# Performance work log

Hardware: AMD Instinct MI355X
Metric: run time of the kernel (lower is better)

Reference implementation:

```python
import jax, jax.numpy as jnp
import numpy as np

NUM_HEADS = 4
NUM_LEVELS = 4
NUM_POINTS = 8
EMBED = 256
HEAD_DIM = EMBED // NUM_HEADS
SHAPES = np.array([[92, 160], [46, 80], [23, 40], [12, 20]], dtype=np.int64)  # (h, w) per level
NUM_VALUE = int((SHAPES[:, 0] * SHAPES[:, 1]).sum())  # 19560
DEPTH = 64
NQ = 20000
BS = 1
NZ = 4  # num_Z_anchors; NUM_POINTS % NZ == 0


def _depth_bias():
    # replicates init_smpl_off_weights for sampling_offsets_depth.bias
    th = np.arange(NUM_HEADS) * (2.0 * np.pi / NUM_HEADS)
    g = ((np.cos(th) + np.sin(th)) / 2.0)[:, None, None] * np.ones((NUM_HEADS, NUM_LEVELS, NUM_POINTS))
    g = g * (np.arange(NUM_POINTS) + 1)[None, None, :]
    return jnp.asarray(g.reshape(-1), dtype=jnp.float32)


def setup_inputs() -> dict:
    key = jax.random.key(0)
    ks = jax.random.split(key, 8)
    f = jnp.float32
    s = 0.02
    query = jax.random.normal(ks[0], (BS, NQ, EMBED), f)
    value = jax.random.normal(ks[1], (BS, NUM_VALUE, EMBED), f)
    value_dpt_dist = jax.nn.softmax(jax.random.normal(ks[2], (BS, NUM_VALUE, DEPTH), f), axis=-1)
    reference_points = jax.random.uniform(ks[3], (BS, NQ, NZ, 3), f)
    spatial_shapes = jnp.asarray(SHAPES)
    level_start_index = jnp.asarray(np.concatenate([[0], np.cumsum(SHAPES[:, 0] * SHAPES[:, 1])[:-1]]))
    Wv = jax.random.normal(ks[4], (EMBED, EMBED), f) * s
    bv = jnp.zeros((EMBED,), f)
    Wo = jax.random.normal(ks[5], (EMBED, NUM_HEADS * NUM_LEVELS * NUM_POINTS * 2), f) * s
    bo = jax.random.normal(ks[6], (NUM_HEADS * NUM_LEVELS * NUM_POINTS * 2,), f) * 0.5
    Wod = jnp.zeros((EMBED, NUM_HEADS * NUM_LEVELS * NUM_POINTS), f)  # constant_init 0.0
    bod = _depth_bias()
    Wa = jax.random.normal(ks[7], (EMBED, NUM_HEADS * NUM_LEVELS * NUM_POINTS), f) * s
    ba = jnp.zeros((NUM_HEADS * NUM_LEVELS * NUM_POINTS,), f)
    return dict(query=query, value=value, value_dpt_dist=value_dpt_dist,
                reference_points=reference_points, spatial_shapes=spatial_shapes,
                level_start_index=level_start_index, Wv=Wv, bv=bv, Wo=Wo, bo=bo,
                Wod=Wod, bod=bod, Wa=Wa, ba=ba)


def _forward(query, value, value_dpt_dist, reference_points, spatial_shapes,
             level_start_index, Wv, bv, Wo, bo, Wod, bod, Wa, ba):
    bs, nq, _ = query.shape
    H, L, P = NUM_HEADS, NUM_LEVELS, NUM_POINTS
    dh = HEAD_DIM
    D = value_dpt_dist.shape[-1]
    dt = query.dtype
    shapes = np.asarray(spatial_shapes)  # static level shapes

    v = (value @ Wv + bv).reshape(bs, -1, H, dh)  # value_proj
    off_uv = (query @ Wo + bo).reshape(bs, nq, H, L, P, 2)
    off_d = (query @ Wod + bod).reshape(bs, nq, H, L, P, 1)
    off = jnp.concatenate([off_uv, off_d], axis=-1)  # (bs,nq,H,L,P,3)
    attn = jax.nn.softmax((query @ Wa + ba).reshape(bs, nq, H, L * P), axis=-1)
    attn = attn.reshape(bs, nq, H, L, P)

    # offset_normalizer = (w, h, D) per level
    norm = jnp.asarray(np.stack([shapes[:, 1], shapes[:, 0], np.full(L, D)], -1), dtype=dt)
    off = off / norm[None, None, None, :, None, :]
    Z = reference_points.shape[2]
    off = off.reshape(bs, nq, H, L, P // Z, Z, 3)
    loc = (reference_points[:, :, None, None, None, :, :] + off).reshape(bs, nq, H, L, P, 3)

    starts = np.concatenate([[0], np.cumsum(shapes[:, 0] * shapes[:, 1])]).astype(int)
    gather_bh = jax.vmap(jax.vmap(lambda a, i: a[i]))   # over (bs, heads)
    gather_b = jax.vmap(lambda a, i: a[i])              # over bs

    out = jnp.zeros((bs, nq, H, dh), dt)
    for l in range(L):
        Hl, Wl = int(shapes[l, 0]), int(shapes[l, 1])
        v_l = v[:, starts[l]:starts[l + 1]].transpose(0, 2, 1, 3)          # (bs,H,HW,dh)
        d_l = value_dpt_dist[:, starts[l]:starts[l + 1]].reshape(bs, Hl * Wl * D)
        ll = loc[:, :, :, l]                                               # (bs,nq,H,P,3)
        # grid_sample (align_corners=False) pixel coordinates
        x = ll[..., 0] * Wl - 0.5
        y = ll[..., 1] * Hl - 0.5
        z = ll[..., 2] * D - 0.5
        x0f, y0f, z0f = jnp.floor(x), jnp.floor(y), jnp.floor(z)
        fx, fy, fz = x - x0f, y - y0f, z - z0f
        x0 = x0f.astype(jnp.int32); y0 = y0f.astype(jnp.int32); z0 = z0f.astype(jnp.int32)
        z0c = jnp.clip(z0, 0, D - 1)
        z1c = jnp.clip(z0 + 1, 0, D - 1)
        wz0 = (1.0 - fz) * ((z0 >= 0) & (z0 <= D - 1)).astype(dt)
        wz1 = fz * ((z0 + 1 >= 0) & (z0 + 1 <= D - 1)).astype(dt)

        acc = jnp.zeros((bs, nq, H, P, dh), dt)
        for xi, wx in ((x0, 1.0 - fx), (x0 + 1, fx)):
            for yi, wy in ((y0, 1.0 - fy), (y0 + 1, fy)):
                valid = ((xi >= 0) & (xi < Wl) & (yi >= 0) & (yi < Hl)).astype(dt)
                w_uv = wx * wy * valid                                     # (bs,nq,H,P)
                idx = jnp.clip(yi, 0, Hl - 1) * Wl + jnp.clip(xi, 0, Wl - 1)
                idx_h = idx.transpose(0, 2, 1, 3).reshape(bs, H, nq * P)
                val = gather_bh(v_l, idx_h).reshape(bs, H, nq, P, dh).transpose(0, 2, 1, 3, 4)
                d0 = gather_b(d_l, (idx * D + z0c).reshape(bs, -1)).reshape(bs, nq, H, P)
                d1 = gather_b(d_l, (idx * D + z1c).reshape(bs, -1)).reshape(bs, nq, H, P)
                dscore = wz0 * d0 + wz1 * d1                               # depth lerp at this spatial corner
                acc = acc + (w_uv * dscore)[..., None] * val
        out = out + jnp.einsum('bqhp,bqhpd->bqhd', attn[:, :, :, l], acc)
    return out.reshape(bs, nq, H * dh)


def reference(query, value, value_dpt_dist, reference_points, spatial_shapes,
              level_start_index, Wv, bv, Wo, bo, Wod, bod, Wa, ba):
    return _forward(query, value, value_dpt_dist, reference_points, spatial_shapes,
                    level_start_index, Wv, bv, Wo, bo, Wod, bod, Wa, ba)
```

## Files before the change

kernel.cpp:

```cpp
#include <hip/hip_runtime.h>
#include <math.h>

#define NQ    20000
#define NV    19560
#define NHEAD 4
#define DEPTHD 64

typedef __attribute__((ext_vector_type(8))) short short8;
typedef __attribute__((ext_vector_type(4))) float f32x4;

__device__ __forceinline__ ushort f2bf(float f) {
    uint32_t u = __float_as_uint(f);
    uint32_t r = (u + 0x7FFFu + ((u >> 16) & 1u)) >> 16;
    return (ushort)r;
}
__device__ __forceinline__ float bf_lo(uint32_t d) { return __uint_as_float(d << 16); }
__device__ __forceinline__ float bf_hi(uint32_t d) { return __uint_as_float(d & 0xFFFF0000u); }

__global__ __launch_bounds__(256) void prep_weights(
    const float* __restrict__ Wv, const float* __restrict__ Wo,
    const float* __restrict__ Wod, const float* __restrict__ Wa,
    const float* __restrict__ bo, const float* __restrict__ bod,
    const float* __restrict__ ba,
    ushort* __restrict__ WvT, ushort* __restrict__ WqT, float* __restrict__ bq)
{
    const int b = blockIdx.x;
    const int k = threadIdx.x;
    if (b < 256) {
        WvT[b * 256 + k] = f2bf(Wv[k * 256 + b]);
    } else if (b < 768) {
        const int n = b - 256;
        float w;
        if (n < 256)      w = Wo [k * 256 + n];
        else if (n < 384) w = Wod[k * 128 + (n - 256)];
        else              w = Wa [k * 128 + (n - 384)];
        WqT[n * 256 + k] = f2bf(w);
    } else {
        for (int i = k; i < 512; i += 256) {
            float v;
            if (i < 256)      v = bo[i];
            else if (i < 384) v = bod[i - 256];
            else              v = ba[i - 384];
            bq[i] = v;
        }
    }
}

__global__ __launch_bounds__(256) void prep_dd4(
    const float* __restrict__ dd, uint2* __restrict__ dd4)
{
    __shared__ float tile[33][65];
    const int r0 = blockIdx.x * 32;
    for (int i = threadIdx.x; i < 33 * 64; i += 256) {
        const int rr = i >> 6, zz = i & 63;
        const int gr = min(r0 + rr, NV - 1);
        tile[rr][zz] = dd[(size_t)gr * 64 + zz];
    }
    __syncthreads();
    for (int i = threadIdx.x; i < 32 * 64; i += 256) {
        const int zz = i >> 5;
        const int rr = i & 31;
        if (r0 + rr < NV) {
            const int z1 = min(zz + 1, 63);
            uint2 o;
            o.x = (uint32_t)f2bf(tile[rr][zz])     | ((uint32_t)f2bf(tile[rr][z1])     << 16);
            o.y = (uint32_t)f2bf(tile[rr + 1][zz]) | ((uint32_t)f2bf(tile[rr + 1][z1]) << 16);
            dd4[(size_t)zz * NV + r0 + rr] = o;
        }
    }
}

template<bool BF16_OUT>
__global__ __launch_bounds__(256) void gemm_mfma_bf16(
    const float* __restrict__ A, const ushort* __restrict__ BT,
    const float* __restrict__ bias, void* __restrict__ Cout,
    int M, int ldc)
{
    constexpr int K = 256, BK = 32;
    __shared__ ushort Asb[128][40];
    __shared__ ushort Bsb[128][40];

    const int tid  = threadIdx.x;
    const int lane = tid & 63;
    const int wave = tid >> 6;
    const int wm   = wave >> 1;
    const int wn   = wave & 1;
    const int brow = blockIdx.y * 128;
    const int bcol = blockIdx.x * 128;
    const int l15  = lane & 15;
    const int kg   = lane >> 4;

    f32x4 acc[4][4] = {};

    const int rA    = tid >> 1;
    const int partA = tid & 1;

    for (int k0 = 0; k0 < K; k0 += BK) {
        {
            ushort tmp[16];
            if (brow + rA < M) {
                const float* ap = A + (size_t)(brow + rA) * K + k0 + partA * 16;
                #pragma unroll
                for (int i = 0; i < 4; ++i) {
                    float4 v = *reinterpret_cast<const float4*>(ap + i * 4);
                    tmp[i * 4 + 0] = f2bf(v.x);
                    tmp[i * 4 + 1] = f2bf(v.y);
                    tmp[i * 4 + 2] = f2bf(v.z);
                    tmp[i * 4 + 3] = f2bf(v.w);
                }
            } else {
                #pragma unroll
                for (int i = 0; i < 16; ++i) tmp[i] = 0;
            }
            *reinterpret_cast<uint4*>(&Asb[rA][partA * 16 + 0]) = *reinterpret_cast<uint4*>(tmp);
            *reinterpret_cast<uint4*>(&Asb[rA][partA * 16 + 8]) = *reinterpret_cast<uint4*>(tmp + 8);
        }
        #pragma unroll
        for (int i = 0; i < 2; ++i) {
            int f  = tid + i * 256;
            int n  = f >> 2;
            int c8 = (f & 3) * 8;
            uint4 v = *reinterpret_cast<const uint4*>(BT + (size_t)(bcol + n) * K + k0 + c8);
            *reinterpret_cast<uint4*>(&Bsb[n][c8]) = v;
        }
        __syncthreads();

        short8 af[4], bfv[4];
        #pragma unroll
        for (int mf = 0; mf < 4; ++mf)
            af[mf] = *reinterpret_cast<const short8*>(&Asb[wm * 64 + mf * 16 + l15][kg * 8]);
        #pragma unroll
        for (int nf = 0; nf < 4; ++nf)
            bfv[nf] = *reinterpret_cast<const short8*>(&Bsb[wn * 64 + nf * 16 + l15][kg * 8]);
        #pragma unroll
        for (int mf = 0; mf < 4; ++mf)
            #pragma unroll
            for (int nf = 0; nf < 4; ++nf)
                acc[mf][nf] = __builtin_amdgcn_mfma_f32_16x16x32_bf16(af[mf], bfv[nf], acc[mf][nf], 0, 0, 0);
        __syncthreads();
    }

    #pragma unroll
    for (int mf = 0; mf < 4; ++mf) {
        #pragma unroll
        for (int reg = 0; reg < 4; ++reg) {
            int row = brow + wm * 64 + mf * 16 + kg * 4 + reg;
            if (row >= M) continue;
            #pragma unroll
            for (int nf = 0; nf < 4; ++nf) {
                int col = bcol + wn * 64 + nf * 16 + l15;
                float v = acc[mf][nf][reg] + bias[col];
                if (BF16_OUT)
                    ((ushort*)Cout)[(size_t)row * ldc + col] = f2bf(v);
                else
                    ((float*)Cout)[(size_t)row * ldc + col] = v;
            }
        }
    }
}

__device__ __forceinline__ void fma8(float* acc, float w, uint4 r) {
    acc[0] = fmaf(w, bf_lo(r.x), acc[0]);
    acc[1] = fmaf(w, bf_hi(r.x), acc[1]);
    acc[2] = fmaf(w, bf_lo(r.y), acc[2]);
    acc[3] = fmaf(w, bf_hi(r.y), acc[3]);
    acc[4] = fmaf(w, bf_lo(r.z), acc[4]);
    acc[5] = fmaf(w, bf_hi(r.z), acc[5]);
    acc[6] = fmaf(w, bf_lo(r.w), acc[6]);
    acc[7] = fmaf(w, bf_hi(r.w), acc[7]);
}

__global__ __launch_bounds__(256, 2) void deform_sample(
    const float* __restrict__ qproj,
    const ushort* __restrict__ vproj,
    const uint2* __restrict__ dd4,
    const float* __restrict__ refpts,
    float* __restrict__ out)
{
    const int b    = blockIdx.x;
    const int h    = threadIdx.x >> 6;
    const int lane = threadIdx.x & 63;
    const int j    = lane & 31;
    const int qq   = lane >> 5;
    const int q    = 2 * b + qq;

    __shared__ uint32_t smoff [NHEAD][2][128];
    __shared__ float    smcoef[NHEAD][2][128];

    const float* qrow = qproj + (size_t)q * 512;

    const float logit = qrow[384 + h * 32 + j];

    const int l  = j >> 3;
    const int p  = j & 7;
    const int zi = p & 3;
    const int Wl = 160 >> l;
    const int Hl = (l == 0) ? 92 : (l == 1) ? 46 : (l == 2) ? 23 : 12;
    const int st = (l == 0) ? 0  : (l == 1) ? 14720 : (l == 2) ? 18400 : 19320;

    const int oidx = (h * 4 + l) * 8 + p;
    const float ox = qrow[oidx * 2 + 0];
    const float oy = qrow[oidx * 2 + 1];
    const float od = qrow[256 + oidx];
    const float rx = refpts[(q * 4 + zi) * 3 + 0];
    const float ry = refpts[(q * 4 + zi) * 3 + 1];
    const float rz = refpts[(q * 4 + zi) * 3 + 2];

    const float x = fmaf(rx, (float)Wl, ox - 0.5f);
    const float y = fmaf(ry, (float)Hl, oy - 0.5f);
    const float z = fmaf(rz, 64.0f,     od - 0.5f);
    const float x0f = floorf(x), y0f = floorf(y), z0f = floorf(z);
    const float fx = x - x0f, fy = y - y0f, fz = z - z0f;
    const int x0 = (int)x0f, y0 = (int)y0f, z0 = (int)z0f;

    const int z0c = min(max(z0, 0), DEPTHD - 1);
    const float wlo = (z0 >= 0 && z0 <= 63) ? (1.f - fz) : ((z0 == -1) ? fz : 0.f);
    const float whi = (z0 >= 0 && z0 <= 62) ? fz : 0.f;

    const int yc0 = min(max(y0, 0), Hl - 1);
    const int yc1 = min(max(y0 + 1, 0), Hl - 1);
    const int xb  = min(max(x0, 0), Wl - 2);
    const int xc0 = min(max(x0, 0), Wl - 1);
    const int xc1 = min(max(x0 + 1, 0), Wl - 1);
    const int s0i = xc0 - xb;
    const int s1i = xc1 - xb;

    const uint2* plane = dd4 + (size_t)z0c * NV + st + xb;
    const uint2 u0 = plane[yc0 * Wl];
    const uint2 u1 = plane[yc1 * Wl];

    const int r00 = st + yc0 * Wl + xc0;
    const int r01 = st + yc0 * Wl + xc1;
    const int r10 = st + yc1 * Wl + xc0;
    const int r11 = st + yc1 * Wl + xc1;
    smoff[h][qq][0 * 32 + j] = (uint32_t)(r00 * 512 + h * 128);
    smoff[h][qq][1 * 32 + j] = (uint32_t)(r01 * 512 + h * 128);
    smoff[h][qq][2 * 32 + j] = (uint32_t)(r10 * 512 + h * 128);
    smoff[h][qq][3 * 32 + j] = (uint32_t)(r11 * 512 + h * 128);

    const int g   = lane >> 3;
    const int ch8 = (lane & 7) << 3;
    const uint32_t chb = (uint32_t)(ch8 << 1);
    const char* vb = (const char*)vproj;
    const uint32_t* o0 = smoff[h][0];
    const uint32_t* o1 = smoff[h][1];

    uint4 rA[8], rB[8];
    #pragma unroll
    for (int t = 0; t < 8; ++t)
        rA[t] = *reinterpret_cast<const uint4*>(vb + (o0[t * 8 + g] + chb));
    #pragma unroll
    for (int t = 0; t < 8; ++t)
        rB[t] = *reinterpret_cast<const uint4*>(vb + (o1[t * 8 + g] + chb));

    float m = logit;
    #pragma unroll
    for (int o = 16; o; o >>= 1) m = fmaxf(m, __shfl_xor(m, o));
    float e = __expf(logit - m);
    float s = e;
    #pragma unroll
    for (int o = 16; o; o >>= 1) s += __shfl_xor(s, o);
    const float aw = e / s;

    const float wx0 = 1.f - fx, wx1 = fx;
    const float wy0 = 1.f - fy, wy1 = fy;
    const bool vx0 = (x0 >= 0) & (x0 < Wl);
    const bool vx1 = (x0 + 1 >= 0) & (x0 + 1 < Wl);
    const bool vy0 = (y0 >= 0) & (y0 < Hl);
    const bool vy1 = (y0 + 1 >= 0) & (y0 + 1 < Hl);

    const uint32_t pd00 = s0i ? u0.y : u0.x;
    const uint32_t pd01 = s1i ? u0.y : u0.x;
    const uint32_t pd10 = s0i ? u1.y : u1.x;
    const uint32_t pd11 = s1i ? u1.y : u1.x;

    const float ds00 = wlo * bf_lo(pd00) + whi * bf_hi(pd00);
    const float ds01 = wlo * bf_lo(pd01) + whi * bf_hi(pd01);
    const float ds10 = wlo * bf_lo(pd10) + whi * bf_hi(pd10);
    const float ds11 = wlo * bf_lo(pd11) + whi * bf_hi(pd11);
    smcoef[h][qq][0 * 32 + j] = (vx0 && vy0) ? (aw * wx0 * wy0 * ds00) : 0.f;
    smcoef[h][qq][1 * 32 + j] = (vx1 && vy0) ? (aw * wx1 * wy0 * ds01) : 0.f;
    smcoef[h][qq][2 * 32 + j] = (vx0 && vy1) ? (aw * wx0 * wy1 * ds10) : 0.f;
    smcoef[h][qq][3 * 32 + j] = (vx1 && vy1) ? (aw * wx1 * wy1 * ds11) : 0.f;

    const float* c0 = smcoef[h][0];
    const float* c1 = smcoef[h][1];

    float acc0[8] = {}, acc1[8] = {};
    #pragma unroll
    for (int t = 0; t < 8; ++t) {
        fma8(acc0, c0[t * 8 + g], rA[t]);
        rA[t] = *reinterpret_cast<const uint4*>(vb + (o0[(t + 8) * 8 + g] + chb));
    }
    #pragma unroll
    for (int t = 0; t < 8; ++t) {
        fma8(acc1, c1[t * 8 + g], rB[t]);
        rB[t] = *reinterpret_cast<const uint4*>(vb + (o1[(t + 8) * 8 + g] + chb));
    }
    #pragma unroll
    for (int t = 0; t < 8; ++t) fma8(acc0, c0[(t + 8) * 8 + g], rA[t]);
    #pragma unroll
    for (int t = 0; t < 8; ++t) fma8(acc1, c1[(t + 8) * 8 + g], rB[t]);

    #pragma unroll
    for (int o = 8; o <= 32; o <<= 1) {
        #pragma unroll
        for (int k = 0; k < 8; ++k) {
            acc0[k] += __shfl_xor(acc0[k], o);
            acc1[k] += __shfl_xor(acc1[k], o);
        }
    }

    if (g == 0) {
        float* op0 = out + (size_t)(2 * b) * 256 + h * 64 + ch8;
        f32x4 o00 = {acc0[0], acc0[1], acc0[2], acc0[3]};
        f32x4 o01 = {acc0[4], acc0[5], acc0[6], acc0[7]};
        __builtin_nontemporal_store(o00, reinterpret_cast<f32x4*>(op0));
        __builtin_nontemporal_store(o01, reinterpret_cast<f32x4*>(op0 + 4));
        float* op1 = op0 + 256;
        f32x4 o10 = {acc1[0], acc1[1], acc1[2], acc1[3]};
        f32x4 o11 = {acc1[4], acc1[5], acc1[6], acc1[7]};
        __builtin_nontemporal_store(o10, reinterpret_cast<f32x4*>(op1));
        __builtin_nontemporal_store(o11, reinterpret_cast<f32x4*>(op1 + 4));
    }
}

extern "C" void kernel_launch(void* const* d_in, const int* in_sizes, int n_in,
                              void* d_out, int out_size, void* d_ws, size_t ws_size,
                              hipStream_t stream)
{
    const float* query  = (const float*)d_in[0];
    const float* value  = (const float*)d_in[1];
    const float* ddist  = (const float*)d_in[2];
    const float* refpts = (const float*)d_in[3];
    const float* Wv  = (const float*)d_in[6];
    const float* bv  = (const float*)d_in[7];
    const float* Wo  = (const float*)d_in[8];
    const float* bo  = (const float*)d_in[9];
    const float* Wod = (const float*)d_in[10];
    const float* bod = (const float*)d_in[11];
    const float* Wa  = (const float*)d_in[12];
    const float* ba  = (const float*)d_in[13];
    float* out = (float*)d_out;

    char* ws = (char*)d_ws;
    ushort* vbuf = (ushort*)ws;
    float*  qbuf = (float*)(ws + 10014720);
    ushort* WvT  = (ushort*)(ws + 10014720 + 40960000);
    ushort* WqT  = WvT + 256 * 256;
    float*  bq   = (float*)(WqT + 512 * 256);
    uint2*  dd4  = (uint2*)((char*)bq + 2048);

    dim3 blk(256);

    prep_weights<<<dim3(769), blk, 0, stream>>>(Wv, Wo, Wod, Wa, bo, bod, ba, WvT, WqT, bq);
    prep_dd4<<<dim3((NV + 31) / 32), blk, 0, stream>>>(ddist, dd4);

    gemm_mfma_bf16<true><<<dim3(2, (NV + 127) / 128), blk, 0, stream>>>(
        value, WvT, bv, vbuf, NV, 256);

    gemm_mfma_bf16<false><<<dim3(4, (NQ + 127) / 128), blk, 0, stream>>>(
        query, WqT, bq, qbuf, NQ, 512);

    deform_sample<<<dim3(NQ / 2), blk, 0, stream>>>(qbuf, vbuf, dd4, refpts, out);
}
```

Before: 152.7 us.

## Merge prep and GEMM launches, serialize per-query sampling for higher occupancy

Folds the weight-transpose and depth-table prep into one launch, and the value and query projection GEMMs into one launch that uses a z grid dimension and early-exits surplus value blocks. This cuts launch count and lets the two independent GEMMs run concurrently. The sampling kernel now processes its two queries one after another with a single register set, and launch bounds go from 2 to 8 blocks per CU to reduce register pressure and raise occupancy. The cost is less memory-level parallelism per wave in the gather phase, and a possible spill if the compiler cannot meet the tighter register budget.

```diff
diff --git a/kernel.cpp b/kernel.cpp
--- a/kernel.cpp
+++ b/kernel.cpp
@@ -17,68 +17,75 @@
 __device__ __forceinline__ float bf_lo(uint32_t d) { return __uint_as_float(d << 16); }
 __device__ __forceinline__ float bf_hi(uint32_t d) { return __uint_as_float(d & 0xFFFF0000u); }
 
-__global__ __launch_bounds__(256) void prep_weights(
+#define PB_DD0 769
+
+__global__ __launch_bounds__(256) void prep_all(
     const float* __restrict__ Wv, const float* __restrict__ Wo,
     const float* __restrict__ Wod, const float* __restrict__ Wa,
     const float* __restrict__ bo, const float* __restrict__ bod,
-    const float* __restrict__ ba,
-    ushort* __restrict__ WvT, ushort* __restrict__ WqT, float* __restrict__ bq)
+    const float* __restrict__ ba, const float* __restrict__ dd,
+    ushort* __restrict__ WvT, ushort* __restrict__ WqT, float* __restrict__ bq,
+    uint2* __restrict__ dd4)
 {
+    __shared__ float tile[33][65];
     const int b = blockIdx.x;
-    const int k = threadIdx.x;
+    const int t = threadIdx.x;
     if (b < 256) {
-        WvT[b * 256 + k] = f2bf(Wv[k * 256 + b]);
+        WvT[b * 256 + t] = f2bf(Wv[t * 256 + b]);
     } else if (b < 768) {
         const int n = b - 256;
         float w;
-        if (n < 256)      w = Wo [k * 256 + n];
-        else if (n < 384) w = Wod[k * 128 + (n - 256)];
-        else              w = Wa [k * 128 + (n - 384)];
-        WqT[n * 256 + k] = f2bf(w);
-    } else {
-        for (int i = k; i < 512; i += 256) {
+        if (n < 256)      w = Wo [t * 256 + n];
+        else if (n < 384) w = Wod[t * 128 + (n - 256)];
+        else              w = Wa [t * 128 + (n - 384)];
+        WqT[n * 256 + t] = f2bf(w);
+    } else if (b == 768) {
+        for (int i = t; i < 512; i += 256) {
             float v;
             if (i < 256)      v = bo[i];
             else if (i < 384) v = bod[i - 256];
             else              v = ba[i - 384];
             bq[i] = v;
         }
-    }
-}
-
-__global__ __launch_bounds__(256) void prep_dd4(
-    const float* __restrict__ dd, uint2* __restrict__ dd4)
-{
-    __shared__ float tile[33][65];
-    const int r0 = blockIdx.x * 32;
-    for (int i = threadIdx.x; i < 33 * 64; i += 256) {
-        const int rr = i >> 6, zz = i & 63;
-        const int gr = min(r0 + rr, NV - 1);
-        tile[rr][zz] = dd[(size_t)gr * 64 + zz];
-    }
-    __syncthreads();
-    for (int i = threadIdx.x; i < 32 * 64; i += 256) {
-        const int zz = i >> 5;
-        const int rr = i & 31;
-        if (r0 + rr < NV) {
-            const int z1 = min(zz + 1, 63);
-            uint2 o;
-            o.x = (uint32_t)f2bf(tile[rr][zz])     | ((uint32_t)f2bf(tile[rr][z1])     << 16);
-            o.y = (uint32_t)f2bf(tile[rr + 1][zz]) | ((uint32_t)f2bf(tile[rr + 1][z1]) << 16);
-            dd4[(size_t)zz * NV + r0 + rr] = o;
-        }
-    }
-}
-
-template<bool BF16_OUT>
-__global__ __launch_bounds__(256) void gemm_mfma_bf16(
-    const float* __restrict__ A, const ushort* __restrict__ BT,
-    const float* __restrict__ bias, void* __restrict__ Cout,
-    int M, int ldc)
+    } else {
+        const int r0 = (b - PB_DD0) * 32;
+        for (int i = t; i < 33 * 64; i += 256) {
+            const int rr = i >> 6, zz = i & 63;
+            const int gr = min(r0 + rr, NV - 1);
+            tile[rr][zz] = dd[(size_t)gr * 64 + zz];
+        }
+        __syncthreads();
+        for (int i = t; i < 32 * 64; i += 256) {
+            const int zz = i >> 5;
+            const int rr = i & 31;
+            if (r0 + rr < NV) {
+                const int z1 = min(zz + 1, 63);
+                uint2 o;
+                o.x = (uint32_t)f2bf(tile[rr][zz])     | ((uint32_t)f2bf(tile[rr][z1])     << 16);
+                o.y = (uint32_t)f2bf(tile[rr + 1][zz]) | ((uint32_t)f2bf(tile[rr + 1][z1]) << 16);
+                dd4[(size_t)zz * NV + r0 + rr] = o;
+            }
+        }
+    }
+}
+
+__global__ __launch_bounds__(256) void gemm_fused(
+    const float* __restrict__ Av, const ushort* __restrict__ BTv,
+    const float* __restrict__ biasv, ushort* __restrict__ Cv,
+    const float* __restrict__ Aq, const ushort* __restrict__ BTq,
+    const float* __restrict__ biasq, float* __restrict__ Cq)
 {
     constexpr int K = 256, BK = 32;
     __shared__ ushort Asb[128][40];
     __shared__ ushort Bsb[128][40];
+
+    const bool isq = (blockIdx.z == 1);
+    if (!isq && (blockIdx.x >= 2 || blockIdx.y >= 153)) return;
+
+    const float*  A    = isq ? Aq : Av;
+    const ushort* BT   = isq ? BTq : BTv;
+    const float*  bias = isq ? biasq : biasv;
+    const int     M    = isq ? NQ : NV;
 
     const int tid  = threadIdx.x;
     const int lane = tid & 63;
@@ -150,10 +157,10 @@
             for (int nf = 0; nf < 4; ++nf) {
                 int col = bcol + wn * 64 + nf * 16 + l15;
                 float v = acc[mf][nf][reg] + bias[col];
-                if (BF16_OUT)
-                    ((ushort*)Cout)[(size_t)row * ldc + col] = f2bf(v);
+                if (isq)
+                    Cq[(size_t)row * 512 + col] = v;
                 else
-                    ((float*)Cout)[(size_t)row * ldc + col] = v;
+                    Cv[(size_t)row * 256 + col] = f2bf(v);
             }
         }
     }
@@ -170,7 +177,7 @@
     acc[7] = fmaf(w, bf_hi(r.w), acc[7]);
 }
 
-__global__ __launch_bounds__(256, 2) void deform_sample(
+__global__ __launch_bounds__(256, 8) void deform_sample(
     const float* __restrict__ qproj,
     const ushort* __restrict__ vproj,
     const uint2* __restrict__ dd4,
@@ -245,13 +252,10 @@
     const uint32_t* o0 = smoff[h][0];
     const uint32_t* o1 = smoff[h][1];
 
-    uint4 rA[8], rB[8];
+    uint4 r[8];
     #pragma unroll
     for (int t = 0; t < 8; ++t)
-        rA[t] = *reinterpret_cast<const uint4*>(vb + (o0[t * 8 + g] + chb));
-    #pragma unroll
-    for (int t = 0; t < 8; ++t)
-        rB[t] = *reinterpret_cast<const uint4*>(vb + (o1[t * 8 + g] + chb));
+        r[t] = *reinterpret_cast<const uint4*>(vb + (o0[t * 8 + g] + chb));
 
     float m = logit;
     #pragma unroll
@@ -286,40 +290,56 @@
     const float* c0 = smcoef[h][0];
     const float* c1 = smcoef[h][1];
 
-    float acc0[8] = {}, acc1[8] = {};
+    float acc[8] = {};
     #pragma unroll
     for (int t = 0; t < 8; ++t) {
-        fma8(acc0, c0[t * 8 + g], rA[t]);
-        rA[t] = *reinterpret_cast<const uint4*>(vb + (o0[(t + 8) * 8 + g] + chb));
-    }
-    #pragma unroll
-    for (int t = 0; t < 8; ++t) {
-        fma8(acc1, c1[t * 8 + g], rB[t]);
-        rB[t] = *reinterpret_cast<const uint4*>(vb + (o1[(t + 8) * 8 + g] + chb));
-    }
-    #pragma unroll
-    for (int t = 0; t < 8; ++t) fma8(acc0, c0[(t + 8) * 8 + g], rA[t]);
-    #pragma unroll
-    for (int t = 0; t < 8; ++t) fma8(acc1, c1[(t + 8) * 8 + g], rB[t]);
-
-    #pragma unroll
-    for (int o = 8; o <= 32; o <<= 1) {
-        #pragma unroll
-        for (int k = 0; k < 8; ++k) {
-            acc0[k] += __shfl_xor(acc0[k], o);
-            acc1[k] += __shfl_xor(acc1[k], o);
-        }
-    }
+        fma8(acc, c0[t * 8 + g], r[t]);
+        r[t] = *reinterpret_cast<const uint4*>(vb + (o0[(t + 8) * 8 + g] + chb));
+    }
+    #pragma unroll
+    for (int t = 0; t < 8; ++t)
+        fma8(acc, c0[(t + 8) * 8 + g], r[t]);
+
+    uint4 r2[8];
+    #pragma unroll
+    for (int t = 0; t < 8; ++t)
+        r2[t] = *reinterpret_cast<const uint4*>(vb + (o1[t * 8 + g] + chb));
+
+    #pragma unroll
+    for (int o = 8; o <= 32; o <<= 1)
+        #pragma unroll
+        for (int k = 0; k < 8; ++k)
+            acc[k] += __shfl_xor(acc[k], o);
 
     if (g == 0) {
         float* op0 = out + (size_t)(2 * b) * 256 + h * 64 + ch8;
-        f32x4 o00 = {acc0[0], acc0[1], acc0[2], acc0[3]};
-        f32x4 o01 = {acc0[4], acc0[5], acc0[6], acc0[7]};
+        f32x4 o00 = {acc[0], acc[1], acc[2], acc[3]};
+        f32x4 o01 = {acc[4], acc[5], acc[6], acc[7]};
         __builtin_nontemporal_store(o00, reinterpret_cast<f32x4*>(op0));
         __builtin_nontemporal_store(o01, reinterpret_cast<f32x4*>(op0 + 4));
-        float* op1 = op0 + 256;
-        f32x4 o10 = {acc1[0], acc1[1], acc1[2], acc1[3]};
-        f32x4 o11 = {acc1[4], acc1[5], acc1[6], acc1[7]};
+    }
+
+    #pragma unroll
+    for (int k = 0; k < 8; ++k) acc[k] = 0.f;
+    #pragma unroll
+    for (int t = 0; t < 8; ++t) {
+        fma8(acc, c1[t * 8 + g], r2[t]);
+        r2[t] = *reinterpret_cast<const uint4*>(vb + (o1[(t + 8) * 8 + g] + chb));
+    }
+    #pragma unroll
+    for (int t = 0; t < 8; ++t)
+        fma8(acc, c1[(t + 8) * 8 + g], r2[t]);
+
+    #pragma unroll
+    for (int o = 8; o <= 32; o <<= 1)
+        #pragma unroll
+        for (int k = 0; k < 8; ++k)
+            acc[k] += __shfl_xor(acc[k], o);
+
+    if (g == 0) {
+        float* op1 = out + (size_t)(2 * b + 1) * 256 + h * 64 + ch8;
+        f32x4 o10 = {acc[0], acc[1], acc[2], acc[3]};
+        f32x4 o11 = {acc[4], acc[5], acc[6], acc[7]};
         __builtin_nontemporal_store(o10, reinterpret_cast<f32x4*>(op1));
         __builtin_nontemporal_store(o11, reinterpret_cast<f32x4*>(op1 + 4));
     }
@@ -353,14 +373,12 @@
 
     dim3 blk(256);
 
-    prep_weights<<<dim3(769), blk, 0, stream>>>(Wv, Wo, Wod, Wa, bo, bod, ba, WvT, WqT, bq);
-    prep_dd4<<<dim3((NV + 31) / 32), blk, 0, stream>>>(ddist, dd4);
-
-    gemm_mfma_bf16<true><<<dim3(2, (NV + 127) / 128), blk, 0, stream>>>(
-        value, WvT, bv, vbuf, NV, 256);
-
-    gemm_mfma_bf16<false><<<dim3(4, (NQ + 127) / 128), blk, 0, stream>>>(
-        query, WqT, bq, qbuf, NQ, 512);
+    const int nDD = (NV + 31) / 32;
+    prep_all<<<dim3(PB_DD0 + nDD), blk, 0, stream>>>(
+        Wv, Wo, Wod, Wa, bo, bod, ba, ddist, WvT, WqT, bq, dd4);
+
+    gemm_fused<<<dim3(4, 157, 2), blk, 0, stream>>>(
+        value, WvT, bv, vbuf, query, WqT, bq, qbuf);
 
     deform_sample<<<dim3(NQ / 2), blk, 0, stream>>>(qbuf, vbuf, dd4, refpts, out);
 }
```

Result: slower. 517.6 us (+239.0%).
